# Optimization experiments

Hardware: AMD Instinct MI355X
Metric: run time of the kernel (lower is better)

The kernel has to match this reference:

```python
import jax, jax.numpy as jnp
import numpy as np

B, S, E, H = 4, 2048, 768, 12
D = E // H  # head dimension = 64


def setup_inputs() -> dict:
    key = jax.random.key(0)
    ks = jax.random.split(key, 10)
    scale = 1.0 / np.sqrt(E)
    x = jax.random.normal(ks[0], (B, S, E), dtype=jnp.float32)
    mask = jax.random.randint(ks[1], (B, S), 0, 2, dtype=jnp.int32)
    # per-head Q/K/V projections stacked over heads: [H, E, D]
    Wq = jax.random.normal(ks[2], (H, E, D), dtype=jnp.float32) * scale
    bq = jax.random.normal(ks[3], (H, D), dtype=jnp.float32) * scale
    Wk = jax.random.normal(ks[4], (H, E, D), dtype=jnp.float32) * scale
    bk = jax.random.normal(ks[5], (H, D), dtype=jnp.float32) * scale
    Wv = jax.random.normal(ks[6], (H, E, D), dtype=jnp.float32) * scale
    bv = jax.random.normal(ks[7], (H, D), dtype=jnp.float32) * scale
    # output projection: [H*D, E]
    Wo = jax.random.normal(ks[8], (H * D, E), dtype=jnp.float32) * scale
    bo = jax.random.normal(ks[9], (E,), dtype=jnp.float32) * scale
    return {"x": x, "mask": mask, "Wq": Wq, "bq": bq, "Wk": Wk, "bk": bk,
            "Wv": Wv, "bv": bv, "Wo": Wo, "bo": bo}


def reference(x, mask, Wq, bq, Wk, bk, Wv, bv, Wo, bo):
    # Per-head linear projections, vectorized over heads: [B, H, S, D]
    q = jnp.einsum('bse,hed->bhsd', x, Wq) + bq[None, :, None, :]
    k = jnp.einsum('bse,hed->bhsd', x, Wk) + bk[None, :, None, :]
    v = jnp.einsum('bse,hed->bhsd', x, Wv) + bv[None, :, None, :]
    # scores: [B, H, S, S]
    scores = jnp.einsum('bhqd,bhkd->bhqk', q, k) / jnp.sqrt(jnp.float32(D))
    # mask [B, S] broadcast over heads and query positions (key-side mask)
    key_mask = mask[:, None, None, :]  # [B, 1, 1, S]
    scores = jnp.where(key_mask == 0, jnp.float32(-1e9), scores)
    attn = jax.nn.softmax(scores, axis=-1)
    out = jnp.einsum('bhqk,bhkd->bhqd', attn, v)  # [B, H, S, D]
    # concat heads: [B, S, H*D]
    out = out.transpose(0, 2, 1, 3).reshape(B, S, H * D)
    return out @ Wo + bo
```

## Files before the change

### kernel.cpp

```cpp
#include <hip/hip_runtime.h>
#include <hip/hip_bf16.h>

#define B_ 4
#define S_ 2048
#define E_ 768
#define H_ 12
#define D_ 64
#define M_ (B_*S_)
#define NQKV 2304
#define KDIM 768

typedef __bf16 bf16x8 __attribute__((ext_vector_type(8)));
typedef float f32x4 __attribute__((ext_vector_type(4)));
typedef short shortx4 __attribute__((ext_vector_type(4)));
typedef unsigned int uintx2 __attribute__((ext_vector_type(2)));
typedef unsigned int uintx4 __attribute__((ext_vector_type(4)));

typedef __attribute__((address_space(1))) void gvoid;
typedef __attribute__((address_space(3))) void lvoid;

__device__ __forceinline__ void gl_lds16(const void* g, void* l) {
  __builtin_amdgcn_global_load_lds((gvoid*)g, (lvoid*)l, 16, 0, 0);
}

__device__ __forceinline__ f32x4 mfma16(bf16x8 a, bf16x8 b, f32x4 c) {
  return __builtin_amdgcn_mfma_f32_16x16x32_bf16(a, b, c, 0, 0, 0);
}

__device__ __forceinline__ f32x4 mfma_pv(shortx4 a, shortx4 b, f32x4 c) {
#if __has_builtin(__builtin_amdgcn_mfma_f32_16x16x16bf16_1k)
  return __builtin_amdgcn_mfma_f32_16x16x16bf16_1k(a, b, c, 0, 0, 0);
#else
  uintx2 au = __builtin_bit_cast(uintx2, a);
  uintx2 bu = __builtin_bit_cast(uintx2, b);
  uintx4 aw = {au.x, au.y, 0u, 0u};
  uintx4 bw = {bu.x, bu.y, 0u, 0u};
  return mfma16(__builtin_bit_cast(bf16x8, aw), __builtin_bit_cast(bf16x8, bw), c);
#endif
}

__device__ __forceinline__ __bf16 ldmix(const void* p, size_t idx, int is_bf) {
  if (is_bf) return ((const __bf16*)p)[idx];
  return (__bf16)(((const float*)p)[idx]);
}
__device__ __forceinline__ float ldmixf(const void* p, size_t idx, int is_bf) {
  if (is_bf) return (float)((const __bf16*)p)[idx];
  return ((const float*)p)[idx];
}

__global__ __launch_bounds__(256) void prep_kernel(
    const void* __restrict__ x, const int* __restrict__ mask,
    const void* __restrict__ Wq, const void* __restrict__ bq,
    const void* __restrict__ Wk, const void* __restrict__ bk,
    const void* __restrict__ Wv, const void* __restrict__ bv,
    const void* __restrict__ Wo, const void* __restrict__ bo,
    int* __restrict__ flag,
    __bf16* __restrict__ Xb,
    __bf16* __restrict__ WbT, __bf16* __restrict__ WoT,
    float* __restrict__ biasP, float* __restrict__ biasO,
    int* __restrict__ R, int* __restrict__ npadArr, int* __restrict__ narrArr)
{
  const int t = threadIdx.x;
  const int bid = blockIdx.x;

  if (bid < 4) {
    __shared__ int wtot[4];
    __shared__ int runningS;
    const int w = t >> 6, lane = t & 63;
    const int b = bid;
    if (t == 0) runningS = 0;
    __syncthreads();
    for (int k0 = 0; k0 < S_; k0 += 256) {
      int keep = (mask[b * S_ + k0 + t] != 0) ? 1 : 0;
      unsigned long long bal = __ballot(keep);
      int lanePre = __popcll(bal & ((1ull << lane) - 1ull));
      if (lane == 0) wtot[w] = __popcll(bal);
      __syncthreads();
      int base = runningS;
      for (int i = 0; i < w; ++i) base += wtot[i];
      if (keep) R[b * S_ + base + lanePre] = b * S_ + k0 + t;
      __syncthreads();
      if (t == 0) runningS += wtot[0] + wtot[1] + wtot[2] + wtot[3];
      __syncthreads();
    }
    int n = runningS;
    for (int j = n + t; j < S_; j += 256)
      R[b * S_ + j] = b * S_;
    if (t == 0) { npadArr[b] = (n + 63) & ~63; narrArr[b] = n; }
    return;
  }

  __shared__ int scnt[4];
  {
    const unsigned short* xr = (const unsigned short*)x;
    unsigned short h = xr[2 * t];
    int e = (h >> 7) & 0xFF;
    unsigned long long bal = __ballot(e >= 100 && e <= 140);
    if ((t & 63) == 0) scnt[t >> 6] = __popcll(bal);
  }
  __syncthreads();
  const int is_bf = (scnt[0] + scnt[1] + scnt[2] + scnt[3] > 148) ? 1 : 0;
  if (bid == 4 && t == 0) *flag = is_bf;

  const int cb = bid - 4;
  if (cb < 3072) {
    int base = (cb * 256 + t) * 8;
    if (is_bf) {
      *(uintx4*)(Xb + base) = *(const uintx4*)((const __bf16*)x + base);
    } else {
      const float* xf = (const float*)x + base;
      f32x4 a = *(const f32x4*)xf;
      f32x4 c = *(const f32x4*)(xf + 4);
      __bf16 ov[8] = {(__bf16)a[0], (__bf16)a[1], (__bf16)a[2], (__bf16)a[3],
                      (__bf16)c[0], (__bf16)c[1], (__bf16)c[2], (__bf16)c[3]};
      *(uintx4*)(Xb + base) = *(uintx4*)ov;
    }
    return;
  }

  const int tb = cb - 3072;
  if (tb >= 577) return;

  if (tb == 576) {
    for (int i = t; i < 3072; i += 256) {
      if (i < NQKV) {
        int sel = i / 768, hd = i - sel * 768;
        const void* bsel = (sel == 0) ? bq : (sel == 1) ? bk : bv;
        biasP[i] = ldmixf(bsel, hd, is_bf);
      } else {
        biasO[i - NQKV] = ldmixf(bo, i - NQKV, is_bf);
      }
    }
    return;
  }

  __shared__ __bf16 tl[64][66];
  const int er  = t >> 2;
  const int cg  = (t & 3) * 16;

  const void* src;
  size_t ibase; int istride;
  __bf16* dst; int n0, c0out;
  if (tb < 432) {
    int combo = tb / 12;
    int e0 = (tb - combo * 12) * 64;
    int sel = combo / 12, h = combo - sel * 12;
    src = (sel == 0) ? Wq : (sel == 1) ? Wk : Wv;
    ibase = (size_t)(h * 768 + e0) * 64;
    istride = 64;
    dst = WbT; n0 = sel * 768 + h * 64; c0out = e0;
  } else {
    int tj = tb - 432;
    int r0 = (tj / 12) * 64;
    int c0 = (tj - (tj / 12) * 12) * 64;
    src = Wo;
    ibase = (size_t)c0 * 768 + r0;
    istride = 768;
    dst = WoT; n0 = r0; c0out = c0;
  }

  {
    size_t off = ibase + (size_t)er * istride + cg;
    if (is_bf) {
      bf16x8 a = *(const bf16x8*)((const __bf16*)src + off);
      bf16x8 bvv = *(const bf16x8*)((const __bf16*)src + off + 8);
      *(bf16x8*)(&tl[er][cg]) = a;
      *(bf16x8*)(&tl[er][cg + 8]) = bvv;
    } else {
      const float* sf = (const float*)src + off;
      f32x4 a = *(const f32x4*)sf;
      f32x4 bvv = *(const f32x4*)(sf + 4);
      f32x4 c = *(const f32x4*)(sf + 8);
      f32x4 d = *(const f32x4*)(sf + 12);
      __bf16 cv[16] = {(__bf16)a[0], (__bf16)a[1], (__bf16)a[2], (__bf16)a[3],
                       (__bf16)bvv[0], (__bf16)bvv[1], (__bf16)bvv[2], (__bf16)bvv[3],
                       (__bf16)c[0], (__bf16)c[1], (__bf16)c[2], (__bf16)c[3],
                       (__bf16)d[0], (__bf16)d[1], (__bf16)d[2], (__bf16)d[3]};
      *(bf16x8*)(&tl[er][cg]) = *(bf16x8*)cv;
      *(bf16x8*)(&tl[er][cg + 8]) = *(bf16x8*)(cv + 8);
    }
  }
  __syncthreads();
  {
    const int dr = t >> 2;
    const int ec = (t & 3) * 16;
    __bf16 ov[16];
#pragma unroll
    for (int j = 0; j < 16; ++j) ov[j] = tl[ec + j][dr];
    __bf16* po = dst + (size_t)(n0 + dr) * 768 + c0out + ec;
    *(uintx4*)po = *(uintx4*)ov;
    *(uintx4*)(po + 8) = *(uintx4*)(ov + 8);
  }
}

__global__ __launch_bounds__(256) void gemm_qkv(
    const __bf16* __restrict__ Xb,
    const __bf16* __restrict__ WbT,
    const float* __restrict__ biasP,
    const int* __restrict__ R,
    const int* __restrict__ npadArr,
    __bf16* __restrict__ Qc,
    __bf16* __restrict__ Kc,
    __bf16* __restrict__ Vc)
{
  __shared__ __align__(16) __bf16 As[128 * 32];
  __shared__ __align__(16) __bf16 Bs[128 * 32];
  const int t = threadIdx.x;
  const int wave = t >> 6, lane = t & 63;
  const int l15 = lane & 15, lq = lane >> 4;
  const int wm = (wave & 1) * 64;
  const int wn = (wave >> 1) * 64;

  const int bid = blockIdx.x;
  int m0, bn0, isQ, b = 0;
  int rowA0, rowA1;
  if (bid < 384) {
    isQ = 1;
    int mi = bid / 6, ni = bid - mi * 6;
    m0 = mi * 128; bn0 = ni * 128;
    rowA0 = m0 + (t >> 2);
    rowA1 = m0 + 64 + (t >> 2);
  } else {
    isQ = 0;
    int r2 = bid - 384;
    b = r2 / 192;
    int rr = r2 - b * 192;
    int mi = rr / 12, ni = rr - mi * 12;
    int np = npadArr[b];
    np = (np < 0) ? 0 : ((np > 2048) ? 2048 : np);
    if (mi * 128 >= np) return;
    m0 = mi * 128;
    bn0 = 768 + ni * 128;
    rowA0 = R[b * S_ + m0 + (t >> 2)] & (M_ - 1);
    rowA1 = R[b * S_ + m0 + 64 + (t >> 2)] & (M_ - 1);
  }
  const int c8 = (t & 3) << 3;
  const int brow0 = bn0 + (t >> 2);
  const int brow1 = bn0 + 64 + (t >> 2);

  const f32x4 z4 = {0.f, 0.f, 0.f, 0.f};
  f32x4 acc[4][4];
#pragma unroll
  for (int i = 0; i < 4; ++i)
#pragma unroll
    for (int j = 0; j < 4; ++j) acc[i][j] = z4;

  for (int k0 = 0; k0 < KDIM; k0 += 32) {
    __syncthreads();
    gl_lds16(Xb + (size_t)rowA0 * KDIM + k0 + c8, As + (size_t)wave * 512);
    gl_lds16(Xb + (size_t)rowA1 * KDIM + k0 + c8, As + (size_t)(2048 + wave * 512));
    gl_lds16(WbT + (size_t)brow0 * KDIM + k0 + c8, Bs + (size_t)wave * 512);
    gl_lds16(WbT + (size_t)brow1 * KDIM + k0 + c8, Bs + (size_t)(2048 + wave * 512));
    __syncthreads();
    bf16x8 af[4], bfr[4];
#pragma unroll
    for (int i = 0; i < 4; ++i) af[i]  = *(const bf16x8*)(As + (wm + i * 16 + l15) * 32 + lq * 8);
#pragma unroll
    for (int j = 0; j < 4; ++j) bfr[j] = *(const bf16x8*)(Bs + (wn + j * 16 + l15) * 32 + lq * 8);
#pragma unroll
    for (int i = 0; i < 4; ++i)
#pragma unroll
      for (int j = 0; j < 4; ++j)
        acc[i][j] = mfma16(af[i], bfr[j], acc[i][j]);
  }

#pragma unroll
  for (int j = 0; j < 4; ++j) {
    if (isQ) {
      int nn = bn0 + wn + j * 16 + l15;
      float bv = biasP[nn];
#pragma unroll
      for (int i = 0; i < 4; ++i) {
        int mbase = m0 + wm + i * 16 + lq * 4;
#pragma unroll
        for (int r = 0; r < 4; ++r)
          Qc[(size_t)(mbase + r) * 768 + nn] = (__bf16)(acc[i][j][r] + bv);
      }
    } else {
      int nn = (bn0 - 768) + wn + j * 16 + l15;
      float bv = biasP[768 + nn];
      const int isK = (nn < 768);
      const int hh = (isK ? nn : nn - 768) >> 6;
      const int d  = nn & 63;
      const size_t bhh = (size_t)(b * H_ + hh);
#pragma unroll
      for (int i = 0; i < 4; ++i) {
        int jbase = m0 + wm + i * 16 + lq * 4;
#pragma unroll
        for (int r = 0; r < 4; ++r) {
          int jj = jbase + r;
          __bf16 ov = (__bf16)(acc[i][j][r] + bv);
          if (isK) Kc[(bhh * 2048 + jj) * 64 + d] = ov;
          else     Vc[(bhh * 512 + (jj >> 2)) * 256 + d * 4 + (jj & 3)] = ov;
        }
      }
    }
  }
}

__global__ __launch_bounds__(256) void gemm_out(
    const __bf16* __restrict__ A,
    const __bf16* __restrict__ WoT,
    const float* __restrict__ biasO,
    void* __restrict__ C,
    const int* __restrict__ flag)
{
  __shared__ __align__(16) __bf16 As[128 * 32];
  __shared__ __align__(16) __bf16 Bs[128 * 32];
  const int obf = *flag;
  const int t = threadIdx.x;
  const int wave = t >> 6, lane = t & 63;
  const int l15 = lane & 15, lq = lane >> 4;
  const int wm = (wave & 1) * 64;
  const int wn = (wave >> 1) * 64;
  const int m0 = blockIdx.x * 128;
  const int n0 = blockIdx.y * 128;
  const int c8 = (t & 3) << 3;
  const int rowA0 = m0 + (t >> 2);
  const int rowA1 = m0 + 64 + (t >> 2);
  const int brow0 = n0 + (t >> 2);
  const int brow1 = n0 + 64 + (t >> 2);

  const f32x4 z4 = {0.f, 0.f, 0.f, 0.f};
  f32x4 acc[4][4];
#pragma unroll
  for (int i = 0; i < 4; ++i)
#pragma unroll
    for (int j = 0; j < 4; ++j) acc[i][j] = z4;

  for (int k0 = 0; k0 < KDIM; k0 += 32) {
    __syncthreads();
    gl_lds16(A + (size_t)rowA0 * KDIM + k0 + c8, As + (size_t)wave * 512);
    gl_lds16(A + (size_t)rowA1 * KDIM + k0 + c8, As + (size_t)(2048 + wave * 512));
    gl_lds16(WoT + (size_t)brow0 * KDIM + k0 + c8, Bs + (size_t)wave * 512);
    gl_lds16(WoT + (size_t)brow1 * KDIM + k0 + c8, Bs + (size_t)(2048 + wave * 512));
    __syncthreads();
    bf16x8 af[4], bfr[4];
#pragma unroll
    for (int i = 0; i < 4; ++i) af[i]  = *(const bf16x8*)(As + (wm + i * 16 + l15) * 32 + lq * 8);
#pragma unroll
    for (int j = 0; j < 4; ++j) bfr[j] = *(const bf16x8*)(Bs + (wn + j * 16 + l15) * 32 + lq * 8);
#pragma unroll
    for (int i = 0; i < 4; ++i)
#pragma unroll
      for (int j = 0; j < 4; ++j)
        acc[i][j] = mfma16(af[i], bfr[j], acc[i][j]);
  }

#pragma unroll
  for (int j = 0; j < 4; ++j) {
    int n = n0 + wn + j * 16 + l15;
    float bv = biasO[n];
#pragma unroll
    for (int i = 0; i < 4; ++i) {
      int mbase = m0 + wm + i * 16 + lq * 4;
#pragma unroll
      for (int r = 0; r < 4; ++r) {
        size_t off = (size_t)(mbase + r) * 768 + n;
        float val = acc[i][j][r] + bv;
        if (obf) ((__bf16*)C)[off] = (__bf16)val;
        else     ((float*)C)[off]  = val;
      }
    }
  }
}

__global__ __launch_bounds__(256) void attn_kernel(
    const __bf16* __restrict__ Qc,
    const __bf16* __restrict__ Kc,
    const __bf16* __restrict__ Vc,
    const int* __restrict__ npadArr,
    const int* __restrict__ narrArr,
    __bf16* __restrict__ Out)
{
  __shared__ __align__(16) __bf16 Ks0[2][64 * 32];
  __shared__ __align__(16) __bf16 Ks1[2][64 * 32];
  __shared__ __align__(16) __bf16 Vt[2][16 * 256];

  const int t = threadIdx.x;
  const int w = t >> 6, lane = t & 63;
  const int l15 = lane & 15, qd = lane >> 4;
  const int bh = blockIdx.y;
  const int b = bh / H_, h = bh - b * H_;
  const int q0 = blockIdx.x * 64;
  int Skv = npadArr[b];
  Skv = (Skv < 0) ? 0 : ((Skv > 2048) ? 2048 : Skv);
  int nb = narrArr[b];
  nb = (nb < 0) ? 0 : ((nb > Skv) ? Skv : nb);

  const __bf16* Qb = Qc + (size_t)b * S_ * E_ + h * 64;
  const __bf16* Kb = Kc + (size_t)bh * 2048 * 64;
  const __bf16* Vg = Vc + (size_t)bh * 512 * 256;

  bf16x8 qf[2];
  {
    int qrow = q0 + w * 16 + l15;
    qf[0] = *(const bf16x8*)(Qb + (size_t)qrow * E_ + qd * 8);
    qf[1] = *(const bf16x8*)(Qb + (size_t)qrow * E_ + 32 + qd * 8);
  }

  const f32x4 z4 = {0.f, 0.f, 0.f, 0.f};
  f32x4 o[4];
#pragma unroll
  for (int dt = 0; dt < 4; ++dt) o[dt] = z4;
  f32x4 ol = z4;

  const short one_bf = (short)0x3F80;
  const shortx4 ones4 = {one_bf, one_bf, one_bf, one_bf};

  const int skey = t >> 2;
  const int sch  = (((t & 3) ^ ((t >> 3) & 3)) * 8);
  const int qsw  = ((qd ^ ((l15 >> 1) & 3)) * 8);
  const float SC = 0.18033688011112042f;

  const int nt = Skv >> 6;
  if (nt > 0) {
    gl_lds16(Kb + (size_t)skey * 64 + sch,      &Ks0[0][w * 512]);
    gl_lds16(Kb + (size_t)skey * 64 + 32 + sch, &Ks1[0][w * 512]);
    gl_lds16(Vg + t * 8,        &Vt[0][w * 512]);
    gl_lds16(Vg + 2048 + t * 8, &Vt[0][2048 + w * 512]);
  }

  for (int ti = 0; ti < nt; ++ti) {
    const int k0 = ti << 6;
    const int cur = ti & 1;
    if (ti + 1 < nt) {
      const int nxt = cur ^ 1;
      const int kk = k0 + 64;
      gl_lds16(Kb + (size_t)(kk + skey) * 64 + sch,      &Ks0[nxt][w * 512]);
      gl_lds16(Kb + (size_t)(kk + skey) * 64 + 32 + sch, &Ks1[nxt][w * 512]);
      const __bf16* vsrc = Vg + ((size_t)(kk >> 2)) * 256;
      gl_lds16(vsrc + t * 8,        &Vt[nxt][w * 512]);
      gl_lds16(vsrc + 2048 + t * 8, &Vt[nxt][2048 + w * 512]);
      asm volatile("s_waitcnt vmcnt(4)" ::: "memory");
    } else {
      asm volatile("s_waitcnt vmcnt(0)" ::: "memory");
    }
    __builtin_amdgcn_s_barrier();

    const __bf16* K0 = Ks0[cur];
    const __bf16* K1 = Ks1[cur];
    const __bf16* Vb = Vt[cur];

    bf16x8 kf[4][2];
#pragma unroll
    for (int kt = 0; kt < 4; ++kt) {
      kf[kt][0] = *(const bf16x8*)(K0 + (kt * 16 + l15) * 32 + qsw);
      kf[kt][1] = *(const bf16x8*)(K1 + (kt * 16 + l15) * 32 + qsw);
    }
    shortx4 vf[4][4];
#pragma unroll
    for (int kt = 0; kt < 4; ++kt)
#pragma unroll
      for (int dt = 0; dt < 4; ++dt)
        vf[kt][dt] = *(const shortx4*)(Vb + (kt * 4 + qd) * 256 + (dt * 16 + l15) * 4);

    f32x4 ma[4];
    if (k0 + 64 <= nb) {
#pragma unroll
      for (int kt = 0; kt < 4; ++kt) ma[kt] = z4;
    } else {
#pragma unroll
      for (int kt = 0; kt < 4; ++kt) {
        int kk = k0 + kt * 16 + qd * 4;
#pragma unroll
        for (int r = 0; r < 4; ++r)
          ma[kt][r] = (kk + r < nb) ? 0.f : -1.0e9f;
      }
    }

    {
      f32x4 s[4];
#pragma unroll
      for (int kt = 0; kt < 4; ++kt) {
        s[kt] = mfma16(kf[kt][0], qf[0], z4);
        s[kt] = mfma16(kf[kt][1], qf[1], s[kt]);
      }
      shortx4 pfr[4];
#pragma unroll
      for (int kt = 0; kt < 4; ++kt) {
        float p0 = __builtin_amdgcn_exp2f(__builtin_fmaf(s[kt][0], SC, ma[kt][0]));
        float p1 = __builtin_amdgcn_exp2f(__builtin_fmaf(s[kt][1], SC, ma[kt][1]));
        float p2 = __builtin_amdgcn_exp2f(__builtin_fmaf(s[kt][2], SC, ma[kt][2]));
        float p3 = __builtin_amdgcn_exp2f(__builtin_fmaf(s[kt][3], SC, ma[kt][3]));
        unsigned int lo16 = __builtin_amdgcn_perm(__builtin_bit_cast(unsigned int, p1),
                                                  __builtin_bit_cast(unsigned int, p0), 0x07060302u);
        unsigned int hi16 = __builtin_amdgcn_perm(__builtin_bit_cast(unsigned int, p3),
                                                  __builtin_bit_cast(unsigned int, p2), 0x07060302u);
        uintx2 u = {lo16, hi16};
        pfr[kt] = __builtin_bit_cast(shortx4, u);
      }
#pragma unroll
      for (int dt = 0; dt < 4; ++dt)
#pragma unroll
        for (int kt = 0; kt < 4; ++kt)
          o[dt] = mfma_pv(pfr[kt], vf[kt][dt], o[dt]);
#pragma unroll
      for (int kt = 0; kt < 4; ++kt)
        ol = mfma_pv(pfr[kt], ones4, ol);
    }

    __builtin_amdgcn_s_barrier();
  }

#pragma unroll
  for (int dt = 0; dt < 4; ++dt)
#pragma unroll
    for (int r = 0; r < 4; ++r) {
      int qrow = q0 + w * 16 + qd * 4 + r;
      Out[(size_t)(b * S_ + qrow) * E_ + h * 64 + dt * 16 + l15] =
          (__bf16)(o[dt][r] / ol[r]);
    }
}

extern "C" void kernel_launch(void* const* d_in, const int* in_sizes, int n_in,
                              void* d_out, int out_size, void* d_ws, size_t ws_size,
                              hipStream_t stream) {
  const void* x  = d_in[0];
  const int* mask = (const int*)d_in[1];
  const void* Wq = d_in[2];
  const void* bq = d_in[3];
  const void* Wk = d_in[4];
  const void* bk = d_in[5];
  const void* Wv = d_in[6];
  const void* bv = d_in[7];
  const void* Wo = d_in[8];
  const void* bo = d_in[9];

  char* ws = (char*)d_ws;
  int*    flag  = (int*)(ws + 0);
  __bf16* Xb    = (__bf16*)(ws + 256);
  __bf16* WbT   = (__bf16*)(ws + 12583168);
  __bf16* WoT   = (__bf16*)(ws + 16122112);
  float*  biasP = (float*)(ws + 17301760);
  float*  biasO = (float*)(ws + 17310976);
  __bf16* Qc    = (__bf16*)(ws + 17314048);
  __bf16* Kc    = (__bf16*)(ws + 29896960);
  __bf16* Vc    = (__bf16*)(ws + 42479872);
  __bf16* attnO = (__bf16*)(ws + 55062784);
  int*    Ridx  = (int*)(ws + 67645696);
  int*    npad  = (int*)(ws + 67711232);
  int*    narr  = (int*)(ws + 67711248);

  prep_kernel<<<dim3(3653), dim3(256), 0, stream>>>(
      x, mask, Wq, bq, Wk, bk, Wv, bv, Wo, bo,
      flag, Xb, WbT, WoT, biasP, biasO, Ridx, npad, narr);
  gemm_qkv<<<dim3(1152), dim3(256), 0, stream>>>(Xb, WbT, biasP, Ridx, npad, Qc, Kc, Vc);
  attn_kernel<<<dim3(32, 48), dim3(256), 0, stream>>>(Qc, Kc, Vc, npad, narr, attnO);
  gemm_out<<<dim3(64, 6), dim3(256), 0, stream>>>(attnO, WoT, biasO, d_out, flag);
}
```

Baseline: 208.1 us.

## Double-buffer LDS tiles in QKV GEMM to overlap global loads with MFMA

Splits the QKV projection GEMM's A and B shared-memory tiles into two buffers. The next k-slice is prefetched with direct global-to-LDS loads while the current slice feeds the MFMAs, and partial vmcnt waits replace the full syncthreads pairs. This is meant to hide global-load latency in the K loop, at the cost of doubling LDS use per block (which may lower occupancy). It also relies on hand-placed waitcnt and barriers being correct for the LDS read-after-write ordering.

```diff
diff --git a/kernel.cpp b/kernel.cpp
--- a/kernel.cpp
+++ b/kernel.cpp
@@ -203,8 +203,8 @@
     __bf16* __restrict__ Kc,
     __bf16* __restrict__ Vc)
 {
-  __shared__ __align__(16) __bf16 As[128 * 32];
-  __shared__ __align__(16) __bf16 Bs[128 * 32];
+  __shared__ __align__(16) __bf16 As[2][128 * 32];
+  __shared__ __align__(16) __bf16 Bs[2][128 * 32];
   const int t = threadIdx.x;
   const int wave = t >> 6, lane = t & 63;
   const int l15 = lane & 15, lq = lane >> 4;
@@ -245,23 +245,41 @@
 #pragma unroll
     for (int j = 0; j < 4; ++j) acc[i][j] = z4;
 
-  for (int k0 = 0; k0 < KDIM; k0 += 32) {
-    __syncthreads();
-    gl_lds16(Xb + (size_t)rowA0 * KDIM + k0 + c8, As + (size_t)wave * 512);
-    gl_lds16(Xb + (size_t)rowA1 * KDIM + k0 + c8, As + (size_t)(2048 + wave * 512));
-    gl_lds16(WbT + (size_t)brow0 * KDIM + k0 + c8, Bs + (size_t)wave * 512);
-    gl_lds16(WbT + (size_t)brow1 * KDIM + k0 + c8, Bs + (size_t)(2048 + wave * 512));
-    __syncthreads();
+  gl_lds16(Xb + (size_t)rowA0 * KDIM + c8, As[0] + (size_t)wave * 512);
+  gl_lds16(Xb + (size_t)rowA1 * KDIM + c8, As[0] + (size_t)(2048 + wave * 512));
+  gl_lds16(WbT + (size_t)brow0 * KDIM + c8, Bs[0] + (size_t)wave * 512);
+  gl_lds16(WbT + (size_t)brow1 * KDIM + c8, Bs[0] + (size_t)(2048 + wave * 512));
+
+  const int NK = KDIM / 32;
+  for (int ki = 0; ki < NK; ++ki) {
+    const int cur = ki & 1;
+    if (ki + 1 < NK) {
+      const int nxt = cur ^ 1;
+      const int k1 = (ki + 1) * 32;
+      gl_lds16(Xb + (size_t)rowA0 * KDIM + k1 + c8, As[nxt] + (size_t)wave * 512);
+      gl_lds16(Xb + (size_t)rowA1 * KDIM + k1 + c8, As[nxt] + (size_t)(2048 + wave * 512));
+      gl_lds16(WbT + (size_t)brow0 * KDIM + k1 + c8, Bs[nxt] + (size_t)wave * 512);
+      gl_lds16(WbT + (size_t)brow1 * KDIM + k1 + c8, Bs[nxt] + (size_t)(2048 + wave * 512));
+      asm volatile("s_waitcnt vmcnt(4)" ::: "memory");
+    } else {
+      asm volatile("s_waitcnt vmcnt(0)" ::: "memory");
+    }
+    __builtin_amdgcn_s_barrier();
+
+    const __bf16* Ab = As[cur];
+    const __bf16* Bb = Bs[cur];
     bf16x8 af[4], bfr[4];
 #pragma unroll
-    for (int i = 0; i < 4; ++i) af[i]  = *(const bf16x8*)(As + (wm + i * 16 + l15) * 32 + lq * 8);
-#pragma unroll
-    for (int j = 0; j < 4; ++j) bfr[j] = *(const bf16x8*)(Bs + (wn + j * 16 + l15) * 32 + lq * 8);
+    for (int i = 0; i < 4; ++i) af[i]  = *(const bf16x8*)(Ab + (wm + i * 16 + l15) * 32 + lq * 8);
+#pragma unroll
+    for (int j = 0; j < 4; ++j) bfr[j] = *(const bf16x8*)(Bb + (wn + j * 16 + l15) * 32 + lq * 8);
 #pragma unroll
     for (int i = 0; i < 4; ++i)
 #pragma unroll
       for (int j = 0; j < 4; ++j)
         acc[i][j] = mfma16(af[i], bfr[j], acc[i][j]);
+
+    __builtin_amdgcn_s_barrier();
   }
 
 #pragma unroll
```

New measurement: 212.8 us. 1.02x slower.
